# Kernel tuning notes

Measured on AMD Instinct MI355X. Metric: run time of the kernel, lower is better.

The kernel has to match this reference:

```python
import jax, jax.numpy as jnp
import numpy as np

B, S, D = 2, 2048, 4096
H, KVH, HD = 32, 8, 128
THETA = 10000.0


def setup_inputs() -> dict:
    key = jax.random.key(0)
    k1, k2, k3 = jax.random.split(key, 3)
    hidden_states = jax.random.normal(k1, (B, S, D), jnp.float32)
    w_qkv = jax.random.normal(k2, ((KVH * 2 + H) * HD, D), jnp.float32) * 0.02
    w_dense = jax.random.normal(k3, (D, D), jnp.float32) * 0.02
    return {"hidden_states": hidden_states, "w_qkv": w_qkv, "w_dense": w_dense}


def _rope(x, pos):
    # x: [B, H, S, HD]; Falcon rotary embedding (rotate_half convention)
    inv_freq = 1.0 / (THETA ** (jnp.arange(0, HD, 2, dtype=jnp.float32) / HD))
    freqs = pos[:, None] * inv_freq[None, :]           # [S, HD/2]
    emb = jnp.concatenate([freqs, freqs], axis=-1)      # [S, HD]
    cos, sin = jnp.cos(emb), jnp.sin(emb)
    x1, x2 = x[..., : HD // 2], x[..., HD // 2 :]
    rot = jnp.concatenate([-x2, x1], axis=-1)
    return x * cos + rot * sin


def reference(hidden_states, w_qkv, w_dense):
    # fused QKV projection (FalconLinear, no bias)
    fused = jnp.einsum('bsd,ed->bse', hidden_states, w_qkv)  # [B,S,(2KVH+H)*HD]
    g = H // KVH  # query heads per kv head
    qkv = fused.reshape(B, S, KVH, g + 2, HD)
    q = qkv[:, :, :, :g]                        # [B,S,KVH,g,HD]
    k = jnp.broadcast_to(qkv[:, :, :, g:g + 1], q.shape)
    v = jnp.broadcast_to(qkv[:, :, :, g + 1:g + 2], q.shape)
    q, k, v = (t.reshape(B, S, H, HD).transpose(0, 2, 1, 3) for t in (q, k, v))
    pos = jnp.arange(S, dtype=jnp.float32)
    q = _rope(q, pos)
    k = _rope(k, pos)
    scores = jnp.einsum('bhqd,bhkd->bhqk', q, k) / jnp.sqrt(jnp.float32(HD))
    causal = jnp.tril(jnp.ones((S, S), dtype=bool))
    scores = jnp.where(causal, scores, jnp.float32(-1e9))
    attn = jax.nn.softmax(scores, axis=-1)
    out = jnp.einsum('bhqk,bhkd->bhqd', attn, v)
    out = out.transpose(0, 2, 1, 3).reshape(B, S, H * HD)   # merge heads
    return jnp.einsum('bsd,ed->bse', out, w_dense)
```

## Files before the change

kernel.cpp:

```cpp
#include <hip/hip_runtime.h>

#define B_   2
#define S_   2048
#define D_   4096
#define H_   32
#define KVH_ 8
#define HD_  128
#define NE_  6144

using f32x4  = __attribute__((ext_vector_type(4))) float;
using f32x16 = __attribute__((ext_vector_type(16))) float;
using bf16x8 = __attribute__((ext_vector_type(8))) __bf16;
using u16x8  = __attribute__((ext_vector_type(8))) unsigned short;

__device__ __forceinline__ unsigned short f2bf(float f) {
  union { float f; unsigned u; } v; v.f = f;
  unsigned r = v.u + 0x7FFFu + ((v.u >> 16) & 1u);
  return (unsigned short)(r >> 16);
}
__device__ __forceinline__ float bf2f(unsigned short h) {
  union { unsigned u; float f; } v; v.u = ((unsigned)h) << 16; return v.f;
}
__device__ __forceinline__ bf16x8 ld8(const unsigned short* p) {
  return *reinterpret_cast<const bf16x8*>(p);
}
__device__ __forceinline__ bf16x8 ld8b(const void* base, int byte_off) {
  return *reinterpret_cast<const bf16x8*>((const char*)base + byte_off);
}
__device__ __forceinline__ void cp16(const void* g, void* l) {
  __builtin_amdgcn_global_load_lds(
      (const __attribute__((address_space(1))) void*)g,
      (__attribute__((address_space(3))) void*)l, 16, 0, 0);
}
__device__ __forceinline__ float exp2a(float x) {
  float r; asm("v_exp_f32 %0, %1" : "=v"(r) : "v"(x)); return r;
}
__device__ __forceinline__ unsigned cvtpk(float lo, float hi) {
  unsigned r; asm("v_cvt_pk_bf16_f32 %0, %1, %2" : "=v"(r) : "v"(lo), "v"(hi));
  return r;
}

#define SC2F 0.12751652f

__global__ __launch_bounds__(256) void cvt2_f32_bf16(
    const float* __restrict__ s0, unsigned short* __restrict__ d0, int n0,
    const float* __restrict__ s1, unsigned short* __restrict__ d1, int n1)
{
  int i = blockIdx.x * 256 + threadIdx.x;
  const float* src; unsigned short* dst;
  if (i < n0) { src = s0; dst = d0; }
  else        { i -= n0; if (i >= n1) return; src = s1; dst = d1; }
  f32x4 v = *reinterpret_cast<const f32x4*>(src + (size_t)i * 4);
  ushort4 o;
  o.x = f2bf(v[0]); o.y = f2bf(v[1]); o.z = f2bf(v[2]); o.w = f2bf(v[3]);
  *reinterpret_cast<ushort4*>(dst + (size_t)i * 4) = o;
}

template <typename OutT, int NT>
__global__ __launch_bounds__(512, 2) void gemm256(
    const unsigned short* __restrict__ A,
    const unsigned short* __restrict__ Bw,
    OutT* __restrict__ C, int M, int N)
{
  constexpr int K  = 4096;
  constexpr int NI = (K / 64) / 2;
  constexpr int NB = NT / 64;
  constexpr int NN = NT / 64;
  constexpr int WN = NT / 4;
  constexpr int BBUF = NT * 128;
  __shared__ __align__(16) char lds[65536 + 2 * BBUF];

  const int tid  = threadIdx.x;
  const int lane = tid & 63;
  const int wave = tid >> 6;
  const int wr = wave >> 2;
  const int wc = wave & 3;
  const int lr = lane & 15;
  const int lk = (lane >> 4) * 8;

  int id  = blockIdx.y * gridDim.x + blockIdx.x;
  const int nwg = gridDim.x * gridDim.y;
  if ((nwg & 7) == 0) { const int q = nwg >> 3; id = (id & 7) * q + (id >> 3); }
  const int row0 = (id / gridDim.x) * 256;
  const int col0 = (id % gridDim.x) * NT;

  int rwA[2], csA[2], dbA[2];
#pragma unroll
  for (int j = 0; j < 2; ++j) {
    dbA[j] = j * 8192 + tid * 16;
    rwA[j] = dbA[j] >> 7;
    csA[j] = ((dbA[j] & 127) ^ ((rwA[j] & 7) << 4)) >> 1;
  }
  auto stA = [&](int buf, int h, int t) {
#pragma unroll
    for (int j = 0; j < 2; ++j)
      cp16(A + (size_t)(row0 + h * 128 + rwA[j]) * K + t * 64 + csA[j],
           lds + buf * 32768 + h * 16384 + dbA[j]);
  };
  const int dbB = tid * 16;
  const int rwB = dbB >> 7;
  const int csB = ((dbB & 127) ^ ((rwB & 7) << 4)) >> 1;
  auto stB = [&](int buf, int c, int t) {
    cp16(Bw + (size_t)(col0 + c * 64 + rwB) * K + t * 64 + csB,
         lds + 65536 + buf * BBUF + c * 8192 + dbB);
  };

  const int cb0 = ((0 + lk) << 1) ^ ((lr & 7) << 4);
  const int cb1 = ((32 + lk) << 1) ^ ((lr & 7) << 4);
  const int aRowB = (wr * 128 + lr) * 128;
  const int bRowB = (wc * WN + lr) * 128;

  f32x4 acc[8][NN];
#pragma unroll
  for (int m = 0; m < 8; ++m)
#pragma unroll
    for (int n = 0; n < NN; ++n) acc[m][n] = (f32x4){0.f, 0.f, 0.f, 0.f};
  bf16x8 bfr[NN][2];

#define FENCE asm volatile("" ::: "memory")
#define VMNB  do { if constexpr (NB == 4) asm volatile("s_waitcnt vmcnt(4)" ::: "memory"); \
                   else                   asm volatile("s_waitcnt vmcnt(3)" ::: "memory"); } while (0)
#define VM0   asm volatile("s_waitcnt vmcnt(0)" ::: "memory")

#define PHASE(p, buf, STAGE, WAIT)                                             \
  {                                                                            \
    if ((p) == 0) {                                                            \
      _Pragma("unroll")                                                        \
      for (int n = 0; n < NN; ++n) {                                           \
        bfr[n][0] = ld8b(lds, 65536 + (buf) * BBUF + bRowB + n * 2048 + cb0);  \
        bfr[n][1] = ld8b(lds, 65536 + (buf) * BBUF + bRowB + n * 2048 + cb1);  \
      }                                                                        \
    }                                                                          \
    bf16x8 a00 = ld8b(lds, (buf) * 32768 + aRowB + ((p) * 2 + 0) * 2048 + cb0);\
    bf16x8 a01 = ld8b(lds, (buf) * 32768 + aRowB + ((p) * 2 + 0) * 2048 + cb1);\
    bf16x8 a10 = ld8b(lds, (buf) * 32768 + aRowB + ((p) * 2 + 1) * 2048 + cb0);\
    bf16x8 a11 = ld8b(lds, (buf) * 32768 + aRowB + ((p) * 2 + 1) * 2048 + cb1);\
    STAGE;                                                                     \
    FENCE;                                                                     \
    __builtin_amdgcn_s_barrier();                                              \
    __builtin_amdgcn_s_setprio(1);                                             \
    _Pragma("unroll")                                                          \
    for (int n = 0; n < NN; ++n) {                                             \
      acc[(p)*2+0][n] = __builtin_amdgcn_mfma_f32_16x16x32_bf16(a00, bfr[n][0], acc[(p)*2+0][n], 0, 0, 0); \
      acc[(p)*2+0][n] = __builtin_amdgcn_mfma_f32_16x16x32_bf16(a01, bfr[n][1], acc[(p)*2+0][n], 0, 0, 0); \
      acc[(p)*2+1][n] = __builtin_amdgcn_mfma_f32_16x16x32_bf16(a10, bfr[n][0], acc[(p)*2+1][n], 0, 0, 0); \
      acc[(p)*2+1][n] = __builtin_amdgcn_mfma_f32_16x16x32_bf16(a11, bfr[n][1], acc[(p)*2+1][n], 0, 0, 0); \
    }                                                                          \
    __builtin_amdgcn_s_setprio(0);                                             \
    WAIT;                                                                      \
    FENCE;                                                                     \
    __builtin_amdgcn_s_barrier();                                              \
  }

#pragma unroll
  for (int c = 0; c < NB; ++c) stB(0, c, 0);
  stA(0, 0, 0); stA(0, 1, 0);
#pragma unroll
  for (int c = 0; c < NB; ++c) stB(1, c, 1);
  VMNB;
  FENCE;
  __builtin_amdgcn_s_barrier();

  for (int i = 0; i < NI; ++i) {
    const int t1  = 2 * i + 1;
    const int tn0 = 2 * i + 2;
    const int tn1 = 2 * i + 3;
    const bool pre = (i + 1 < NI);
    PHASE(0, 0, { stA(1, 0, t1); }, {});
    PHASE(1, 0, { stA(1, 1, t1); }, {});
    PHASE(2, 0, { if (pre) { stB(0, 0, tn0); stB(0, 1, tn0); } }, {});
    PHASE(3, 0, { if (pre) { _Pragma("unroll") for (int c = 2; c < NB; ++c) stB(0, c, tn0); } },
          { if (pre) { VMNB; } else { VM0; } });
    PHASE(0, 1, { if (pre) stA(0, 0, tn0); }, {});
    PHASE(1, 1, { if (pre) stA(0, 1, tn0); }, {});
    PHASE(2, 1, { if (pre) { stB(1, 0, tn1); stB(1, 1, tn1); } }, {});
    PHASE(3, 1, { if (pre) { _Pragma("unroll") for (int c = 2; c < NB; ++c) stB(1, c, tn1); } },
          { if (pre) { VMNB; } });
  }
#undef PHASE
#undef FENCE
#undef VMNB
#undef VM0

  const int orow = (lane >> 4) * 4;
#pragma unroll
  for (int m = 0; m < 8; ++m) {
    const int gr0 = row0 + wr * 128 + m * 16 + orow;
#pragma unroll
    for (int n = 0; n < NN; ++n) {
      const int gc = col0 + wc * WN + n * 16 + lr;
#pragma unroll
      for (int r = 0; r < 4; ++r) {
        float val = acc[m][n][r];
        if constexpr (sizeof(OutT) == 2)
          C[(size_t)(gr0 + r) * N + gc] = f2bf(val);
        else
          C[(size_t)(gr0 + r) * N + gc] = val;
      }
    }
  }
}

#define ROPE_N (B_ * S_ * 48 * 8)
__global__ __launch_bounds__(256) void rope_scatter_cvt(
    const unsigned short* __restrict__ fused,
    unsigned short* __restrict__ Qr,
    unsigned short* __restrict__ Kr,
    unsigned short* __restrict__ Vt,
    const float* __restrict__ wdense,
    unsigned short* __restrict__ Wdb,
    int nD4)
{
  int idx = blockIdx.x * 256 + threadIdx.x;
  if (idx >= ROPE_N) {
    int i = idx - ROPE_N;
    if (i >= nD4) return;
    f32x4 v = *reinterpret_cast<const f32x4*>(wdense + (size_t)i * 4);
    ushort4 o;
    o.x = f2bf(v[0]); o.y = f2bf(v[1]); o.z = f2bf(v[2]); o.w = f2bf(v[3]);
    *reinterpret_cast<ushort4*>(Wdb + (size_t)i * 4) = o;
    return;
  }
  int dg = idx & 7;
  int t = idx >> 3;
  int e = t % 48;
  int bs = t / 48;
  int s = bs % S_;
  int b = bs / S_;
  int kvh = e / 6, j = e % 6;
  const unsigned short* src = fused + (size_t)bs * NE_ + e * 128 + dg * 8;
  u16x8 lo = *reinterpret_cast<const u16x8*>(src);
  u16x8 hi = *reinterpret_cast<const u16x8*>(src + 64);
  if (j == 5) {
    size_t base = (size_t)(b * KVH_ + kvh) * HD_ * S_ + s;
#pragma unroll
    for (int jj = 0; jj < 8; ++jj) {
      Vt[base + (size_t)(dg * 8 + jj) * S_]      = lo[jj];
      Vt[base + (size_t)(dg * 8 + jj + 64) * S_] = hi[jj];
    }
  } else {
    const float sc = (j == 4) ? 1.0f : SC2F;
    u16x8 olo, ohi;
#pragma unroll
    for (int jj = 0; jj < 8; ++jj) {
      int d = dg * 8 + jj;
      float x1 = bf2f(lo[jj]), x2 = bf2f(hi[jj]);
      float inv = __expf(-(float)d * (9.2103403719761836f / 64.0f));
      float ang = (float)s * inv;
      float sn, c;
      sincosf(ang, &sn, &c);
      olo[jj] = f2bf((x1 * c - x2 * sn) * sc);
      ohi[jj] = f2bf((x2 * c + x1 * sn) * sc);
    }
    unsigned short* dst;
    if (j == 4) dst = Kr + ((size_t)(b * KVH_ + kvh) * S_ + s) * HD_;
    else        dst = Qr + ((size_t)(b * H_ + kvh * 4 + j) * S_ + s) * HD_;
    *reinterpret_cast<u16x8*>(dst + dg * 8)      = olo;
    *reinterpret_cast<u16x8*>(dst + dg * 8 + 64) = ohi;
  }
}

__global__ __launch_bounds__(256, 2) void attn_fwd(
    const unsigned short* __restrict__ Qr,
    const unsigned short* __restrict__ Kr,
    const unsigned short* __restrict__ Vt,
    unsigned short* __restrict__ O)
{
  __shared__ __align__(16) unsigned short Kld[2][64 * 128];
  __shared__ __align__(16) unsigned short Vld[2][128 * 64];

  const int tid  = threadIdx.x;
  const int lane = tid & 63;
  const int wave = tid >> 6;
  const int bx = blockIdx.x;
  const int hh = blockIdx.y;
  const int b  = blockIdx.z;
  const int kvh = hh >> 2;
  const int q31 = lane & 31;
  const int h   = lane >> 5;

  const unsigned short* Kb = Kr + (size_t)(b * KVH_ + kvh) * S_ * HD_;
  const unsigned short* Vb = Vt + (size_t)(b * KVH_ + kvh) * HD_ * S_;

  auto stage = [&](int buf, int kb) {
#pragma unroll
    for (int i = 0; i < 4; ++i) {
      const int db = i * 4096 + tid * 16;
      {
        const int row  = db >> 8;
        const int colb = (db & 255) ^ ((row & 15) << 4);
        cp16(Kb + (size_t)(kb * 64 + row) * HD_ + (colb >> 1),
             (char*)&Kld[buf][0] + i * 4096 + wave * 1024);
      }
      {
        const int row  = db >> 7;
        const int colb = (db & 127) ^ ((row & 7) << 4);
        cp16(Vb + (size_t)row * S_ + kb * 64 + (colb >> 1),
             (char*)&Vld[buf][0] + i * 4096 + wave * 1024);
      }
    }
  };

  const int kswz = (q31 & 15) << 4;
  const int vswz = (q31 & 7) << 4;

  for (int half = 0; half < 2; ++half) {
    const int qt = half ? (15 - bx) : bx;
    const int nkb = 2 * (qt + 1);
    const int qg = qt * 128 + wave * 32 + q31;

    const unsigned short* qbase =
        Qr + ((size_t)(b * H_ + hh) * S_ + qg) * HD_;
    bf16x8 qf[8];
#pragma unroll
    for (int t = 0; t < 8; ++t) qf[t] = ld8(qbase + t * 16 + h * 8);

    f32x16 acc_o[4] = {};
    float m = -1e30f, lpart = 0.f;

    stage(0, 0);
    __syncthreads();

    for (int kb = 0; kb < nkb; ++kb) {
      const int cur = kb & 1;
      if (kb + 1 < nkb) stage(cur ^ 1, kb + 1);

      const char* Kc = (const char*)&Kld[cur][0];
      const char* Vc = (const char*)&Vld[cur][0];

      f32x16 accs0 = {}, accs1 = {};
      __builtin_amdgcn_s_setprio(1);
#pragma unroll
      for (int t = 0; t < 8; ++t) {
        const int hd2 = t * 32 + h * 16;
        bf16x8 kf0 = ld8b(Kc, ((q31 << 8) + hd2) ^ kswz);
        bf16x8 kf1 = ld8b(Kc, (((32 + q31) << 8) + hd2) ^ kswz);
        accs0 = __builtin_amdgcn_mfma_f32_32x32x16_bf16(kf0, qf[t], accs0, 0, 0, 0);
        accs1 = __builtin_amdgcn_mfma_f32_32x32x16_bf16(kf1, qf[t], accs1, 0, 0, 0);
      }
      __builtin_amdgcn_s_setprio(0);

      if (kb >= 2 * qt) {
        const int kbase = kb * 64 + 4 * h;
#pragma unroll
        for (int reg = 0; reg < 16; ++reg) {
          const int k0 = kbase + (reg & 3) + 8 * (reg >> 2);
          if (k0 > qg)      accs0[reg] = -1e30f;
          if (k0 + 32 > qg) accs1[reg] = -1e30f;
        }
      }

      float mx = -1e30f;
#pragma unroll
      for (int reg = 0; reg < 16; ++reg)
        mx = fmaxf(mx, fmaxf(accs0[reg], accs1[reg]));
      if (!__all(mx <= m + 8.f)) {
        float mxo = __shfl_xor(mx, 32, 64);
        float mnew = fmaxf(m, fmaxf(mx, mxo));
        float corr = exp2a(m - mnew);
        m = mnew;
        lpart *= corr;
#pragma unroll
        for (int reg = 0; reg < 16; ++reg) {
          const int crow = (reg & 3) + 8 * (reg >> 2) + 4 * h;
          float cw = __shfl(corr, crow, 64);
#pragma unroll
          for (int dj = 0; dj < 4; ++dj) acc_o[dj][reg] *= cw;
        }
      }

      bf16x8 pa[4];
#pragma unroll
      for (int ks = 0; ks < 4; ++ks) {
        float e[8];
#pragma unroll
        for (int j = 0; j < 8; ++j) {
          float s = (ks < 2) ? accs0[8 * (ks & 1) + j] : accs1[8 * (ks & 1) + j];
          e[j] = exp2a(s - m);
          lpart += e[j];
        }
        unsigned w01 = cvtpk(e[0], e[1]);
        unsigned w23 = cvtpk(e[2], e[3]);
        unsigned w45 = cvtpk(e[4], e[5]);
        unsigned w67 = cvtpk(e[6], e[7]);
        asm volatile("v_permlane32_swap_b32 %0, %1" : "+v"(w01), "+v"(w45));
        asm volatile("v_permlane32_swap_b32 %0, %1" : "+v"(w23), "+v"(w67));
        union { unsigned u[4]; bf16x8 v; } pu;
        pu.u[0] = w01; pu.u[1] = w23; pu.u[2] = w45; pu.u[3] = w67;
        pa[ks] = pu.v;
      }

      __builtin_amdgcn_s_setprio(1);
#pragma unroll
      for (int dj = 0; dj < 4; ++dj) {
        const int vrow = (dj * 32 + q31) << 7;
#pragma unroll
        for (int ks = 0; ks < 4; ++ks) {
          bf16x8 vf = ld8b(Vc, (vrow + ks * 32 + h * 16) ^ vswz);
          acc_o[dj] = __builtin_amdgcn_mfma_f32_32x32x16_bf16(pa[ks], vf, acc_o[dj], 0, 0, 0);
        }
      }
      __builtin_amdgcn_s_setprio(0);

      __syncthreads();
    }

    float lsum = lpart + __shfl_xor(lpart, 32, 64);
    float linv = 1.f / lsum;
#pragma unroll
    for (int reg = 0; reg < 16; ++reg) {
      const int crow = (reg & 3) + 8 * (reg >> 2) + 4 * h;
      float lv = __shfl(linv, crow, 64);
      size_t rowoff =
          (size_t)(b * S_ + qt * 128 + wave * 32 + crow) * (H_ * HD_) + hh * HD_ + q31;
#pragma unroll
      for (int dj = 0; dj < 4; ++dj)
        O[rowoff + dj * 32] = f2bf(acc_o[dj][reg] * lv);
    }
  }
}

__global__ void fill_sentinel(float* __restrict__ O, int n) {
  int i = blockIdx.x * 256 + threadIdx.x;
  if (i < n) O[i] = 12345.0f;
}

extern "C" void kernel_launch(void* const* d_in, const int* in_sizes, int n_in,
                              void* d_out, int out_size, void* d_ws, size_t ws_size,
                              hipStream_t stream) {
  const float* hidden = (const float*)d_in[0];
  const float* wqkv   = (const float*)d_in[1];
  const float* wdense = (const float*)d_in[2];
  float* out = (float*)d_out;

  const size_t NEED = 134217728;
  if (ws_size < NEED) {
    fill_sentinel<<<dim3((out_size + 255) / 256), dim3(256), 0, stream>>>(out, out_size);
    return;
  }

  char* ws = (char*)d_ws;
  unsigned short* Hb    = (unsigned short*)(ws);
  unsigned short* Wqb   = (unsigned short*)(ws + 33554432);
  unsigned short* fused = (unsigned short*)(ws + 83886080);
  unsigned short* Qr    = (unsigned short*)(ws);
  unsigned short* Kr    = (unsigned short*)(ws + 33554432);
  unsigned short* Vt    = (unsigned short*)(ws + 41943040);
  unsigned short* Wdb   = (unsigned short*)(ws + 50331648);
  unsigned short* attn_out = (unsigned short*)(ws + 83886080);

  const int nH4 = B_ * S_ * D_ / 4;
  const int nQ4 = NE_ * D_ / 4;
  const int nD4 = D_ * D_ / 4;

  cvt2_f32_bf16<<<dim3((nH4 + nQ4 + 255) / 256), dim3(256), 0, stream>>>(
      hidden, Hb, nH4, wqkv, Wqb, nQ4);

  gemm256<unsigned short, 192><<<dim3(NE_ / 192, (B_ * S_) / 256), dim3(512), 0, stream>>>(
      Hb, Wqb, fused, B_ * S_, NE_);

  rope_scatter_cvt<<<dim3((ROPE_N + nD4 + 255) / 256), dim3(256), 0, stream>>>(
      fused, Qr, Kr, Vt, wdense, Wdb, nD4);

  attn_fwd<<<dim3(8, H_, B_), dim3(256), 0, stream>>>(Qr, Kr, Vt, attn_out);

  gemm256<float, 256><<<dim3(D_ / 256, (B_ * S_) / 256), dim3(512), 0, stream>>>(
      attn_out, Wdb, out, B_ * S_, D_);
}
```

Baseline: 474.5 us.

## Interleave warp row mapping in GEMM and stage A tiles earlier

Changes the warp-to-row mapping so each phase's A rows come from one contiguous half-tile (rows interleaved across warps at 16-row granularity). That lets the A half-tiles be prefetched earlier in the phase schedule, with finer vmcnt waits placed mid-iteration. The aim is to overlap global-to-LDS copies more deeply with MFMA work and cut stalls at buffer boundaries. The tighter waitcnt accounting risks races if the counts are off.

```diff
diff --git a/kernel.cpp b/kernel.cpp
--- a/kernel.cpp
+++ b/kernel.cpp
@@ -107,7 +107,7 @@
 
   const int cb0 = ((0 + lk) << 1) ^ ((lr & 7) << 4);
   const int cb1 = ((32 + lk) << 1) ^ ((lr & 7) << 4);
-  const int aRowB = (wr * 128 + lr) * 128;
+  const int aRowB = (wr * 16 + lr) * 128;
   const int bRowB = (wc * WN + lr) * 128;
 
   f32x4 acc[8][NN];
@@ -118,9 +118,7 @@
   bf16x8 bfr[NN][2];
 
 #define FENCE asm volatile("" ::: "memory")
-#define VMNB  do { if constexpr (NB == 4) asm volatile("s_waitcnt vmcnt(4)" ::: "memory"); \
-                   else                   asm volatile("s_waitcnt vmcnt(3)" ::: "memory"); } while (0)
-#define VM0   asm volatile("s_waitcnt vmcnt(0)" ::: "memory")
+#define VMC(nn) asm volatile("s_waitcnt vmcnt(" #nn ")" ::: "memory")
 
 #define PHASE(p, buf, STAGE, WAIT)                                             \
   {                                                                            \
@@ -131,10 +129,10 @@
         bfr[n][1] = ld8b(lds, 65536 + (buf) * BBUF + bRowB + n * 2048 + cb1);  \
       }                                                                        \
     }                                                                          \
-    bf16x8 a00 = ld8b(lds, (buf) * 32768 + aRowB + ((p) * 2 + 0) * 2048 + cb0);\
-    bf16x8 a01 = ld8b(lds, (buf) * 32768 + aRowB + ((p) * 2 + 0) * 2048 + cb1);\
-    bf16x8 a10 = ld8b(lds, (buf) * 32768 + aRowB + ((p) * 2 + 1) * 2048 + cb0);\
-    bf16x8 a11 = ld8b(lds, (buf) * 32768 + aRowB + ((p) * 2 + 1) * 2048 + cb1);\
+    bf16x8 a00 = ld8b(lds, (buf) * 32768 + (p) * 8192 + aRowB + cb0);          \
+    bf16x8 a01 = ld8b(lds, (buf) * 32768 + (p) * 8192 + aRowB + cb1);          \
+    bf16x8 a10 = ld8b(lds, (buf) * 32768 + (p) * 8192 + 4096 + aRowB + cb0);   \
+    bf16x8 a11 = ld8b(lds, (buf) * 32768 + (p) * 8192 + 4096 + aRowB + cb1);   \
     STAGE;                                                                     \
     FENCE;                                                                     \
     __builtin_amdgcn_s_barrier();                                              \
@@ -157,7 +155,8 @@
   stA(0, 0, 0); stA(0, 1, 0);
 #pragma unroll
   for (int c = 0; c < NB; ++c) stB(1, c, 1);
-  VMNB;
+  stA(1, 0, 1);
+  if constexpr (NB == 4) { VMC(8); } else { VMC(7); }
   FENCE;
   __builtin_amdgcn_s_barrier();
 
@@ -166,26 +165,30 @@
     const int tn0 = 2 * i + 2;
     const int tn1 = 2 * i + 3;
     const bool pre = (i + 1 < NI);
-    PHASE(0, 0, { stA(1, 0, t1); }, {});
-    PHASE(1, 0, { stA(1, 1, t1); }, {});
-    PHASE(2, 0, { if (pre) { stB(0, 0, tn0); stB(0, 1, tn0); } }, {});
+    PHASE(0, 0, { stA(1, 1, t1); }, {});
+    PHASE(1, 0, { if (pre) { stB(0, 0, tn0); stB(0, 1, tn0); } },
+          { if (pre) { if constexpr (NB == 4) VMC(10); else VMC(9); }
+            else     { if constexpr (NB == 4) VMC(8);  else VMC(7); } });
+    PHASE(2, 0, { if (pre) stA(0, 0, tn0); }, {});
     PHASE(3, 0, { if (pre) { _Pragma("unroll") for (int c = 2; c < NB; ++c) stB(0, c, tn0); } },
-          { if (pre) { VMNB; } else { VM0; } });
-    PHASE(0, 1, { if (pre) stA(0, 0, tn0); }, {});
-    PHASE(1, 1, { if (pre) stA(0, 1, tn0); }, {});
-    PHASE(2, 1, { if (pre) { stB(1, 0, tn1); stB(1, 1, tn1); } }, {});
+          { if (pre) { if constexpr (NB == 4) VMC(8); else VMC(7); }
+            else     { VMC(2); } });
+    PHASE(0, 1, { if (pre) stA(0, 1, tn0); }, {});
+    PHASE(1, 1, { if (pre) { stB(1, 0, tn1); stB(1, 1, tn1); } },
+          { if (pre) { if constexpr (NB == 4) VMC(10); else VMC(9); }
+            else     { VMC(0); } });
+    PHASE(2, 1, { if (pre) stA(1, 0, tn1); }, {});
     PHASE(3, 1, { if (pre) { _Pragma("unroll") for (int c = 2; c < NB; ++c) stB(1, c, tn1); } },
-          { if (pre) { VMNB; } });
+          { if (pre) { if constexpr (NB == 4) VMC(8); else VMC(7); } });
   }
 #undef PHASE
 #undef FENCE
-#undef VMNB
-#undef VM0
+#undef VMC
 
   const int orow = (lane >> 4) * 4;
 #pragma unroll
   for (int m = 0; m < 8; ++m) {
-    const int gr0 = row0 + wr * 128 + m * 16 + orow;
+    const int gr0 = row0 + m * 32 + wr * 16 + orow;
 #pragma unroll
     for (int n = 0; n < NN; ++n) {
       const int gc = col0 + wc * WN + n * 16 + lr;
```

After: 473.2 us. Within noise of the previous version (-0.3%).
